# Performance work log

Measured on AMD Instinct MI355X. Metric: run time of the kernel, lower is better.

Reference implementation:

```python
import jax, jax.numpy as jnp
import numpy as np

DIM = 256
H = 4
K = 16
R = 4
EPS = 1e-5


def _conv1x1(x, W, b):
    # x: [B, Cin, N, P], W: [Cout, Cin], b: [Cout]
    return jnp.einsum('oc,bcnp->bonp', W, x) + b[None, :, None, None]


def setup_inputs() -> dict:
    key = jax.random.key(0)
    ks = jax.random.split(key, 12)
    B, N = 4, 8192
    s = 1.0 / np.sqrt(DIM)
    inp = {
        'queries': jax.random.normal(ks[0], (B, DIM, N, R), dtype=jnp.float32),
        'feats': jax.random.normal(ks[1], (B, DIM, N, K), dtype=jnp.float32),
        'Wq': jax.random.normal(ks[2], (DIM, DIM), dtype=jnp.float32) * s,
        'bq': jnp.zeros((DIM,), dtype=jnp.float32),
        'Wk': jax.random.normal(ks[3], (DIM, DIM), dtype=jnp.float32) * s,
        'bk': jnp.zeros((DIM,), dtype=jnp.float32),
        'Wv': jax.random.normal(ks[4], (DIM, DIM), dtype=jnp.float32) * s,
        'bv': jnp.zeros((DIM,), dtype=jnp.float32),
        'W1': jax.random.normal(ks[5], (2 * DIM, DIM), dtype=jnp.float32) * s,
        'b1': jnp.zeros((2 * DIM,), dtype=jnp.float32),
        'gamma': jnp.ones((2 * DIM,), dtype=jnp.float32),
        'beta': jnp.zeros((2 * DIM,), dtype=jnp.float32),
        'W2': jax.random.normal(ks[6], (DIM, 2 * DIM), dtype=jnp.float32) * (1.0 / np.sqrt(2 * DIM)),
        'b2': jnp.zeros((DIM,), dtype=jnp.float32),
    }
    return inp


def reference(queries, feats, Wq, bq, Wk, bk, Wv, bv, W1, b1, gamma, beta, W2, b2):
    B, _, N, _ = feats.shape
    d = DIM // H
    queries_iden = queries  # [B, dim, N, r]

    q = _conv1x1(queries, Wq, bq).reshape(B, H, d, N, R)   # [B,h,d,N,r]
    k = _conv1x1(feats, Wk, bk).reshape(B, H, d, N, K)     # [B,h,d,N,K]
    v = _conv1x1(feats, Wv, bv).reshape(B, H, d, N, K)     # [B,h,d,N,K]

    # logits: [B,N,h,r,K]
    logits = jnp.einsum('bhdnr,bhdnk->bnhrk', q, k) * (d ** -0.5)
    soft = jax.nn.softmax(logits, axis=-1)
    # agg: [B,N,h,r,d] -> permute to [B,N,h,d,r] -> [B,N,dim,r] -> [B,dim,N,r]
    agg = jnp.einsum('bnhrk,bhdnk->bnhdr', soft, v)
    agg = agg.reshape(B, N, DIM, R).transpose(0, 2, 1, 3)
    agg = agg + queries_iden

    # FFN: conv1x1 -> BN (training-mode batch stats) -> ReLU -> conv1x1, residual, ReLU
    h1 = _conv1x1(agg, W1, b1)  # [B, 2*dim, N, r]
    mean = jnp.mean(h1, axis=(0, 2, 3), keepdims=True)
    var = jnp.var(h1, axis=(0, 2, 3), keepdims=True)
    h1 = (h1 - mean) * jax.lax.rsqrt(var + EPS)
    h1 = h1 * gamma[None, :, None, None] + beta[None, :, None, None]
    h1 = jax.nn.relu(h1)
    h2 = _conv1x1(h1, W2, b2)
    return jax.nn.relu(h2 + agg)
```

## Files before the change

kernel.cpp:

```cpp
#include <hip/hip_runtime.h>
#include <hip/hip_bf16.h>

#define NB 4
#define NRQ 32768
#define NKF 131072

using u16 = unsigned short;
typedef short bf16x8 __attribute__((ext_vector_type(8)));
typedef float f32x4  __attribute__((ext_vector_type(4)));
typedef u16   u16x8  __attribute__((ext_vector_type(8)));
typedef u16   u16x4  __attribute__((ext_vector_type(4)));
typedef u16   u16x2  __attribute__((ext_vector_type(2)));

#if defined(__has_builtin)
#  if __has_builtin(__builtin_amdgcn_fdot2_f32_bf16)
#    define HAVE_DOT2 1
#  endif
#endif
#ifndef HAVE_DOT2
#  define HAVE_DOT2 0
#endif

#if HAVE_DOT2
typedef __bf16 bfv2 __attribute__((ext_vector_type(2)));
union bpack { bf16x8 v; bfv2 p[4]; };
__device__ __forceinline__ float dot2(bfv2 a, bfv2 b, float c){
  return __builtin_amdgcn_fdot2_f32_bf16(a, b, c, false);
}
#endif
union vpack { bf16x8 v; u16 e[8]; };

__device__ __forceinline__ u16 f2b(float f){
  unsigned u = __float_as_uint(f);
  return (u16)((u + 0x7fffu + ((u >> 16) & 1u)) >> 16);
}
__device__ __forceinline__ float b2f(u16 v){
  return __uint_as_float(((unsigned)v) << 16);
}

#define GLOAD16(g, l) __builtin_amdgcn_global_load_lds( \
    (const __attribute__((address_space(1))) unsigned int*)(g), \
    (__attribute__((address_space(3))) unsigned int*)(l), 16, 0, 0)

__global__ __launch_bounds__(256) void cvtW_k(
    const float* __restrict__ Wk, const float* __restrict__ Wv,
    const float* __restrict__ Wq, const float* __restrict__ W1,
    const float* __restrict__ W2, u16* __restrict__ wT)
{
  long e = ((long)blockIdx.x * 256 + threadIdx.x) * 8;
  const float* src; long off;
  if      (e < 65536)  { src = Wk; off = e; }
  else if (e < 131072) { src = Wv; off = e - 65536; }
  else if (e < 196608) { src = Wq; off = e - 131072; }
  else if (e < 327680) { src = W1; off = e - 196608; }
  else                 { src = W2; off = e - 327680; }
  float4 f0 = *reinterpret_cast<const float4*>(src + off);
  float4 f1 = *reinterpret_cast<const float4*>(src + off + 4);
  u16x8 p;
  p[0]=f2b(f0.x); p[1]=f2b(f0.y); p[2]=f2b(f0.z); p[3]=f2b(f0.w);
  p[4]=f2b(f1.x); p[5]=f2b(f1.y); p[6]=f2b(f1.z); p[7]=f2b(f1.w);
  *reinterpret_cast<u16x8*>(wT + e) = p;
}

__global__ void prep_k(const float* __restrict__ bk, const float* __restrict__ bv,
                       float* __restrict__ bKV, float* __restrict__ stats)
{
  int i = blockIdx.x * 256 + threadIdx.x;
  if (i < 512)       bKV[i] = (i < 256) ? bk[i] : bv[i - 256];
  else               stats[i - 512] = 0.f;
}

__global__ __launch_bounds__(256) void transpose_k(
    const float* __restrict__ in, u16* __restrict__ out,
    int NCtot, long outBatch)
{
  __shared__ u16 sT[64][264];
  const int t = threadIdx.x, b = blockIdx.y;
  const int nr0 = blockIdx.x * 64;
  const int cb = t >> 2, nrq = t & 3;
  const long ib = (long)b * 256 * NCtot + nr0;

  #pragma unroll
  for (int ci = 0; ci < 4; ++ci){
    const int c = cb + ci * 64;
    const float* src = in + ib + (long)c * NCtot + nrq * 16;
    #pragma unroll
    for (int j = 0; j < 4; ++j){
      float4 f = *reinterpret_cast<const float4*>(src + j * 4);
      int nr = nrq * 16 + j * 4;
      sT[nr+0][c] = f2b(f.x); sT[nr+1][c] = f2b(f.y);
      sT[nr+2][c] = f2b(f.z); sT[nr+3][c] = f2b(f.w);
    }
  }
  __syncthreads();
  const int row = t >> 2, qtr = t & 3;
  u16* orow = out + (long)b * outBatch + (long)(nr0 + row) * 256 + qtr * 64;
  #pragma unroll
  for (int i = 0; i < 8; ++i)
    *reinterpret_cast<u16x8*>(orow + i * 8) =
        *reinterpret_cast<const u16x8*>(&sT[row][qtr * 64 + i * 8]);
}

template<int MODE, int KD>
__global__ __launch_bounds__(256) void gemm_k(
    const u16* __restrict__ A, long aBatch, int chTiles,
    const u16* __restrict__ Wb, const float* __restrict__ bias,
    u16* __restrict__ outH, long oBatch, int NCH,
    float* __restrict__ statSum, float* __restrict__ statSq,
    const float* __restrict__ xsc, const float* __restrict__ xsh,
    const u16* __restrict__ residT,
    float* __restrict__ outF, long fBatch)
{
  __shared__ __align__(16) char sA[2][16384];
  __shared__ __align__(16) char sB[2][16384];

  const int t = threadIdx.x, lane = t & 63, wid = t >> 6;
  const int wm = wid >> 1, wn = wid & 1;
  const int b = blockIdx.z;

  const int nwg = gridDim.x, orig = blockIdx.x;
  const int qq = nwg >> 3, rr = nwg & 7, xcd = orig & 7, pos = orig >> 3;
  const int wg = (xcd < rr ? xcd * (qq + 1) : rr * (qq + 1) + (xcd - rr) * qq) + pos;
  const int rowT = wg / chTiles, chT = wg % chTiles;

  const u16* Ab = A + (long)b * aBatch + (long)rowT * 128 * KD;
  const u16* Wt = Wb + (long)chT * 128 * KD;
  const int sub = lane >> 3, kc8 = ((lane & 7) ^ sub) * 8;

  f32x4 acc[4][4];
  #pragma unroll
  for (int i = 0; i < 4; ++i)
    #pragma unroll
    for (int j = 0; j < 4; ++j) acc[i][j] = (f32x4){0.f,0.f,0.f,0.f};

  auto STAGE = [&](int buf, int ks){
    const int k0 = ks * 64;
    if constexpr (MODE == 3){
      const int wrow = t >> 1, whalf = t & 1;
      const u16* arow = Ab + (long)wrow * KD + k0 + whalf * 32;
      #pragma unroll
      for (int i = 0; i < 4; ++i){
        u16x8 v = *reinterpret_cast<const u16x8*>(arow + i * 8);
        const int kb = k0 + whalf*32 + i*8;
        float4 s0 = *reinterpret_cast<const float4*>(xsc + kb);
        float4 s1 = *reinterpret_cast<const float4*>(xsc + kb + 4);
        float4 h0 = *reinterpret_cast<const float4*>(xsh + kb);
        float4 h1 = *reinterpret_cast<const float4*>(xsh + kb + 4);
        u16x8 o;
        o[0]=f2b(fmaxf(b2f(v[0])*s0.x+h0.x,0.f));
        o[1]=f2b(fmaxf(b2f(v[1])*s0.y+h0.y,0.f));
        o[2]=f2b(fmaxf(b2f(v[2])*s0.z+h0.z,0.f));
        o[3]=f2b(fmaxf(b2f(v[3])*s0.w+h0.w,0.f));
        o[4]=f2b(fmaxf(b2f(v[4])*s1.x+h1.x,0.f));
        o[5]=f2b(fmaxf(b2f(v[5])*s1.y+h1.y,0.f));
        o[6]=f2b(fmaxf(b2f(v[6])*s1.z+h1.z,0.f));
        o[7]=f2b(fmaxf(b2f(v[7])*s1.w+h1.w,0.f));
        *reinterpret_cast<u16x8*>(
            sA[buf] + ((wrow*128 + whalf*64 + i*16) ^ ((wrow & 7) << 4))) = o;
      }
      #pragma unroll
      for (int i = 0; i < 4; ++i){
        const int chunk = wid * 4 + i;
        GLOAD16(Wt + (long)(chunk*8 + sub)*KD + k0 + kc8, sB[buf] + chunk*1024);
      }
    } else {
      #pragma unroll
      for (int i = 0; i < 4; ++i){
        const int chunk = wid * 4 + i;
        GLOAD16(Ab + (long)(chunk*8 + sub)*KD + k0 + kc8, sA[buf] + chunk*1024);
        GLOAD16(Wt + (long)(chunk*8 + sub)*KD + k0 + kc8, sB[buf] + chunk*1024);
      }
    }
  };

  constexpr int NT = KD / 64;
  STAGE(0, 0);
  __syncthreads();
  int cur = 0;
  for (int ks = 0; ks < NT; ++ks){
    if (ks + 1 < NT) STAGE(cur ^ 1, ks + 1);
    const char* pA = sA[cur]; const char* pB = sB[cur];
    #pragma unroll
    for (int kk = 0; kk < 2; ++kk){
      bf16x8 af[4], bf[4];
      #pragma unroll
      for (int mi = 0; mi < 4; ++mi){
        int m = wm*64 + mi*16 + (lane & 15);
        af[mi] = *reinterpret_cast<const bf16x8*>(
            pA + ((m*128 + kk*64 + (lane>>4)*16) ^ ((m & 7) << 4)));
      }
      #pragma unroll
      for (int ni = 0; ni < 4; ++ni){
        int c = wn*64 + ni*16 + (lane & 15);
        bf[ni] = *reinterpret_cast<const bf16x8*>(
            pB + ((c*128 + kk*64 + (lane>>4)*16) ^ ((c & 7) << 4)));
      }
      #pragma unroll
      for (int mi = 0; mi < 4; ++mi)
        #pragma unroll
        for (int ni = 0; ni < 4; ++ni)
          acc[mi][ni] = __builtin_amdgcn_mfma_f32_16x16x32_bf16(
              af[mi], bf[ni], acc[mi][ni], 0, 0, 0);
    }
    __syncthreads();
    cur ^= 1;
  }

  int chI[4]; float bv[4];
  #pragma unroll
  for (int ni = 0; ni < 4; ++ni){
    int ch = chT*128 + wn*64 + ni*16 + (lane & 15);
    chI[ni] = ch;
    bv[ni] = bias[ch];
  }
  if (MODE <= 1){
    float s[4] = {0,0,0,0}, sq[4] = {0,0,0,0};
    u16* outb = outH + (long)b * oBatch;
    #pragma unroll
    for (int mi = 0; mi < 4; ++mi){
      #pragma unroll
      for (int j = 0; j < 4; ++j){
        const long row = rowT*128 + wm*64 + mi*16 + (lane>>4)*4 + j;
        #pragma unroll
        for (int ni = 0; ni < 4; ++ni){
          float v = acc[mi][ni][j] + bv[ni];
          outb[row * NCH + chI[ni]] = f2b(v);
          if (MODE == 1){ s[ni] += v; sq[ni] += v * v; }
        }
      }
    }
    if (MODE == 1){
      #pragma unroll
      for (int ni = 0; ni < 4; ++ni){
        s[ni]  += __shfl_xor(s[ni], 16);  s[ni]  += __shfl_xor(s[ni], 32);
        sq[ni] += __shfl_xor(sq[ni], 16); sq[ni] += __shfl_xor(sq[ni], 32);
      }
      if (lane < 16){
        #pragma unroll
        for (int ni = 0; ni < 4; ++ni){
          atomicAdd(&statSum[chI[ni]], s[ni]);
          atomicAdd(&statSq[chI[ni]],  sq[ni]);
        }
      }
    }
  } else {
    const u16* rb = residT + (long)b * ((long)NRQ * 256);
    #pragma unroll
    for (int mi = 0; mi < 4; ++mi){
      const int nr0 = rowT*128 + wm*64 + mi*16 + (lane>>4)*4;
      #pragma unroll
      for (int ni = 0; ni < 4; ++ni){
        float4 o;
        o.x = fmaxf(acc[mi][ni][0] + bv[ni] + b2f(rb[(long)(nr0+0)*256 + chI[ni]]), 0.f);
        o.y = fmaxf(acc[mi][ni][1] + bv[ni] + b2f(rb[(long)(nr0+1)*256 + chI[ni]]), 0.f);
        o.z = fmaxf(acc[mi][ni][2] + bv[ni] + b2f(rb[(long)(nr0+2)*256 + chI[ni]]), 0.f);
        o.w = fmaxf(acc[mi][ni][3] + bv[ni] + b2f(rb[(long)(nr0+3)*256 + chI[ni]]), 0.f);
        *reinterpret_cast<float4*>(outF + (long)b*fBatch + (long)chI[ni]*NRQ + nr0) = o;
      }
    }
  }
}

__global__ __launch_bounds__(512, 4) void kvattn_k(
    const float* __restrict__ feats, const u16* __restrict__ wKV,
    const float* __restrict__ bKV, const u16* __restrict__ qT,
    const u16* __restrict__ qrT, u16* __restrict__ aggT)
{
  __shared__ __align__(16) char LDS[73728];
  char*  sAg = LDS;
  char*  sW  = LDS + 8192;
  char*  sK  = LDS;
  char*  sV  = LDS + 33792;
  float* sSf = (float*)(LDS + 67072);

  const int t = threadIdx.x, lane = t & 63, wid = t >> 6;
  const int wr = wid >> 2, wc = wid & 3;
  const int b = blockIdx.y;
  const long row0 = (long)blockIdx.x * 64;

  const int chL = t >> 4, nq = t & 15;
  const float* fbase = feats + (long)b * 256 * NKF + row0 + nq * 4;

  auto STAGEW = [&](int buf, int ks){
    const int k0 = ks * 32;
    #pragma unroll
    for (int i = 0; i < 4; ++i){
      const int cw = wid * 4 + i;
      const int ch = cw * 16 + (lane >> 2), jd = lane & 3;
      GLOAD16(wKV + (long)ch * 256 + k0 + ((jd ^ ((ch >> 1) & 3)) * 8),
              sW + buf * 32768 + cw * 1024);
    }
  };
  auto WRITEA = [&](int buf, float4 f){
    #pragma unroll
    for (int i = 0; i < 4; ++i){
      const int r = nq * 4 + i;
      const int byte = buf*4096 + r*64
                     + (((chL>>3) ^ ((r>>2)&3)) << 4) + (chL & 7)*2;
      float e = (i == 0) ? f.x : (i == 1) ? f.y : (i == 2) ? f.z : f.w;
      *reinterpret_cast<u16*>(sAg + byte) = f2b(e);
    }
  };

  f32x4 acc[2][8];
  #pragma unroll
  for (int i = 0; i < 2; ++i)
    #pragma unroll
    for (int j = 0; j < 8; ++j) acc[i][j] = (f32x4){0.f,0.f,0.f,0.f};

  {
    float4 a0 = *reinterpret_cast<const float4*>(fbase + (long)chL * NKF);
    STAGEW(0, 0);
    WRITEA(0, a0);
  }
  __syncthreads();
  int cur = 0;
  for (int ks = 0; ks < 8; ++ks){
    float4 an;
    if (ks < 7){
      an = *reinterpret_cast<const float4*>(fbase + (long)((ks+1)*32 + chL) * NKF);
      STAGEW(cur ^ 1, ks + 1);
    }
    const char* pA = sAg + cur * 4096;
    const char* pW = sW  + cur * 32768;
    bf16x8 af[2];
    #pragma unroll
    for (int mi = 0; mi < 2; ++mi){
      const int m = wr*32 + mi*16 + (lane & 15);
      af[mi] = *reinterpret_cast<const bf16x8*>(
          pA + m*64 + (((lane>>4) ^ ((m>>2)&3)) * 16));
    }
    #pragma unroll
    for (int ni = 0; ni < 8; ++ni){
      const int ch = wc*128 + ni*16 + (lane & 15);
      bf16x8 bf = *reinterpret_cast<const bf16x8*>(
          pW + ch*64 + (((lane>>4) ^ ((ch>>1)&3)) * 16));
      acc[0][ni] = __builtin_amdgcn_mfma_f32_16x16x32_bf16(af[0], bf, acc[0][ni], 0,0,0);
      acc[1][ni] = __builtin_amdgcn_mfma_f32_16x16x32_bf16(af[1], bf, acc[1][ni], 0,0,0);
    }
    if (ks < 7) WRITEA(cur ^ 1, an);
    __syncthreads();
    cur ^= 1;
  }

  {
    float bv[8];
    #pragma unroll
    for (int ni = 0; ni < 8; ++ni) bv[ni] = bKV[wc*128 + ni*16 + (lane & 15)];
    if (wc < 2){
      #pragma unroll
      for (int mi = 0; mi < 2; ++mi){
        const int p2 = wr*2 + mi;
        #pragma unroll
        for (int ni = 0; ni < 8; ++ni){
          const int ch = wc*128 + ni*16 + (lane & 15);
          #pragma unroll
          for (int j = 0; j < 4; ++j){
            const int kk2 = (lane>>4)*4 + j;
            *reinterpret_cast<u16*>(
                sK + (p2*16 + kk2)*528 + ((ch*2) ^ ((kk2 & 7) << 4))) =
                f2b(acc[mi][ni][j] + bv[ni]);
          }
        }
      }
    } else {
      #pragma unroll
      for (int mi = 0; mi < 2; ++mi){
        const int p2 = wr*2 + mi;
        #pragma unroll
        for (int ni = 0; ni < 8; ++ni){
          const int cv = (wc-2)*128 + ni*16 + (lane & 15);
          #pragma unroll
          for (int j = 0; j < 4; ++j){
            const int kk2 = (lane>>4)*4 + j;
            *reinterpret_cast<u16*>(sV + (p2*16 + kk2)*520 + cv*2) =
                f2b(acc[mi][ni][j] + bv[ni]);
          }
        }
      }
    }
  }
  __syncthreads();

  const int p = wid & 3, rh = wid >> 2;
  const int nqg = blockIdx.x * 4 + p;
  {
    const int h = lane >> 4, kk = lane & 15;
    const u16* qb = qT + ((long)b*NRQ + (long)nqg*4 + rh*2)*256 + h*64;
    const char* kr = sK + (p*16 + kk)*528;
    float l0 = 0.f, l1 = 0.f;
#if HAVE_DOT2
    #pragma unroll
    for (int d8 = 0; d8 < 8; ++d8){
      bpack K8, Q0, Q1;
      K8.v = *reinterpret_cast<const bf16x8*>(
          kr + ((h*128 + d8*16) ^ ((kk & 7) << 4)));
      Q0.v = *reinterpret_cast<const bf16x8*>(qb + d8*8);
      Q1.v = *reinterpret_cast<const bf16x8*>(qb + 256 + d8*8);
      #pragma unroll
      for (int pi = 0; pi < 4; ++pi){
        l0 = dot2(K8.p[pi], Q0.p[pi], l0);
        l1 = dot2(K8.p[pi], Q1.p[pi], l1);
      }
    }
#else
    #pragma unroll
    for (int d8 = 0; d8 < 8; ++d8){
      vpack K8, Q0, Q1;
      K8.v = *reinterpret_cast<const bf16x8*>(
          kr + ((h*128 + d8*16) ^ ((kk & 7) << 4)));
      Q0.v = *reinterpret_cast<const bf16x8*>(qb + d8*8);
      Q1.v = *reinterpret_cast<const bf16x8*>(qb + 256 + d8*8);
      #pragma unroll
      for (int e = 0; e < 8; ++e){
        float kf = b2f(K8.e[e]);
        l0 = fmaf(kf, b2f(Q0.e[e]), l0);
        l1 = fmaf(kf, b2f(Q1.e[e]), l1);
      }
    }
#endif
    float pr[2]; float lv[2] = {l0, l1};
    #pragma unroll
    for (int r = 0; r < 2; ++r){
      float x = lv[r] * 0.125f;
      float m = x;
      #pragma unroll
      for (int off = 1; off < 16; off <<= 1) m = fmaxf(m, __shfl_xor(m, off));
      float e = __expf(x - m);
      float ssum = e;
      #pragma unroll
      for (int off = 1; off < 16; off <<= 1) ssum += __shfl_xor(ssum, off);
      pr[r] = e / ssum;
    }
    *reinterpret_cast<float2*>(sSf + (p*4 + h)*68 + kk*4 + rh*2) =
        make_float2(pr[0], pr[1]);
  }
  __syncthreads();

  {
    const int c0 = rh*128 + lane*2;
    const int h = c0 >> 6;
    const char* vrow = sV + (p*16)*520;
    const float* ss = sSf + (p*4 + h)*68;
    float a[4][2] = {};
    #pragma unroll
    for (int kk = 0; kk < 16; ++kk){
      u16x2 vv = *reinterpret_cast<const u16x2*>(vrow + kk*520 + c0*2);
      float4 sv = *reinterpret_cast<const float4*>(ss + kk*4);
      float v0 = b2f(vv[0]), v1 = b2f(vv[1]);
      a[0][0] += sv.x*v0; a[0][1] += sv.x*v1;
      a[1][0] += sv.y*v0; a[1][1] += sv.y*v1;
      a[2][0] += sv.z*v0; a[2][1] += sv.z*v1;
      a[3][0] += sv.w*v0; a[3][1] += sv.w*v1;
    }
    const u16* rq = qrT + ((long)b*NRQ + (long)nqg*4)*256 + c0;
    u16* ob = aggT + ((long)b*NRQ + (long)nqg*4)*256 + c0;
    #pragma unroll
    for (int r = 0; r < 4; ++r){
      u16x2 q2 = *reinterpret_cast<const u16x2*>(rq + r*256);
      u16x2 pk;
      pk[0] = f2b(a[r][0] + b2f(q2[0]));
      pk[1] = f2b(a[r][1] + b2f(q2[1]));
      *reinterpret_cast<u16x2*>(ob + r*256) = pk;
    }
  }
}

__global__ void finalize_k(const float* __restrict__ st,
                           const float* __restrict__ gamma,
                           const float* __restrict__ beta,
                           float* __restrict__ out)
{
  int o = blockIdx.x*256 + threadIdx.x;
  const float inv = 1.f / 131072.f;
  float mean = st[o] * inv;
  float var  = st[512 + o] * inv - mean*mean;
  float sc   = gamma[o] * rsqrtf(var + 1e-5f);
  out[o]       = sc;
  out[512 + o] = beta[o] - mean * sc;
}

extern "C" void kernel_launch(void* const* d_in, const int* in_sizes, int n_in,
                              void* d_out, int out_size, void* d_ws, size_t ws_size,
                              hipStream_t stream)
{
  (void)in_sizes; (void)n_in; (void)out_size; (void)ws_size;
  const float* queries = (const float*)d_in[0];
  const float* feats   = (const float*)d_in[1];
  const float* Wq = (const float*)d_in[2];
  const float* bq = (const float*)d_in[3];
  const float* Wk = (const float*)d_in[4];
  const float* bk = (const float*)d_in[5];
  const float* Wv = (const float*)d_in[6];
  const float* bv = (const float*)d_in[7];
  const float* W1 = (const float*)d_in[8];
  const float* b1 = (const float*)d_in[9];
  const float* gamma = (const float*)d_in[10];
  const float* beta  = (const float*)d_in[11];
  const float* W2 = (const float*)d_in[12];
  const float* b2 = (const float*)d_in[13];

  char* ws = (char*)d_ws;
  u16*   h1T   = (u16*)ws;
  u16*   qrT   = (u16*)(ws + 134217728L);
  u16*   qT    = (u16*)(ws + 201326592L);
  u16*   aggT  = (u16*)(ws + 268435456L);
  float* stats = (float*)(ws + 335544320L);
  float* scale = stats + 1024;
  float* shift = stats + 1536;
  u16*   wT    = (u16*)(ws + 335552512L);
  u16*   wKV   = wT;
  u16*   wQ    = wT + 131072;
  u16*   wW1   = wT + 196608;
  u16*   wW2   = wT + 327680;
  float* bKV   = (float*)(wT + 458752);

  cvtW_k<<<dim3(224), 256, 0, stream>>>(Wk, Wv, Wq, W1, W2, wT);
  prep_k<<<dim3(6), 256, 0, stream>>>(bk, bv, bKV, stats);

  transpose_k<<<dim3(NRQ/64, NB), 256, 0, stream>>>(queries, qrT, NRQ, (long)NRQ*256);

  gemm_k<0, 256><<<dim3(512, 1, NB), 256, 0, stream>>>(
      qrT, (long)NRQ*256, 2, wQ, bq,
      qT, (long)NRQ*256, 256, nullptr, nullptr, nullptr, nullptr,
      nullptr, nullptr, 0);

  kvattn_k<<<dim3(NKF/64, NB), 512, 0, stream>>>(feats, wKV, bKV, qT, qrT, aggT);

  gemm_k<1, 256><<<dim3(1024, 1, NB), 256, 0, stream>>>(
      aggT, (long)NRQ*256, 4, wW1, b1,
      h1T, (long)NRQ*512, 512, stats, stats + 512, nullptr, nullptr,
      nullptr, nullptr, 0);

  finalize_k<<<dim3(2), 256, 0, stream>>>(stats, gamma, beta, scale);

  gemm_k<3, 512><<<dim3(512, 1, NB), 256, 0, stream>>>(
      h1T, (long)NRQ*512, 2, wW2, b2,
      nullptr, 0, 256, nullptr, nullptr, scale, shift,
      aggT, (float*)d_out, (long)256*NRQ);
}
```

Measured before the change: 649.3 us.

## Stage KV weights through registers with padded LDS, preload Q tile into LDS

Replaces the direct global-to-LDS double-buffered weight staging with register-prefetched loads stored into a single padded LDS buffer. The XOR-swizzled layouts for A, W and K are swapped for padded row strides. The Q rows for the block are loaded once into LDS with an async copy, so the attention step no longer reads them from global memory. In exchange, each k-step gets an extra barrier and register pressure rises. The padded layout uses narrower LDS accesses (4- and 8-byte), which may increase the LDS instruction count.

```diff
diff --git a/kernel.cpp b/kernel.cpp
--- a/kernel.cpp
+++ b/kernel.cpp
@@ -23,12 +23,15 @@
 
 #if HAVE_DOT2
 typedef __bf16 bfv2 __attribute__((ext_vector_type(2)));
-union bpack { bf16x8 v; bfv2 p[4]; };
+union bpack  { bf16x8 v; bfv2 p[4]; };
+union bpack4 { u16x4  v; bfv2 p[2]; };
 __device__ __forceinline__ float dot2(bfv2 a, bfv2 b, float c){
   return __builtin_amdgcn_fdot2_f32_bf16(a, b, c, false);
 }
 #endif
-union vpack { bf16x8 v; u16 e[8]; };
+union vpack  { bf16x8 v; u16 e[8]; };
+union wjoin  { u16x4 h[2]; bf16x8 v; u16x8 u; };
+union ajoin  { unsigned u[4]; bf16x8 v; };
 
 __device__ __forceinline__ u16 f2b(float f){
   unsigned u = __float_as_uint(f);
@@ -266,39 +269,46 @@
     const float* __restrict__ bKV, const u16* __restrict__ qT,
     const u16* __restrict__ qrT, u16* __restrict__ aggT)
 {
-  __shared__ __align__(16) char LDS[73728];
+  __shared__ __align__(16) char LDS[79104];
   char*  sAg = LDS;
-  char*  sW  = LDS + 8192;
+  char*  sW  = LDS + 8704;
   char*  sK  = LDS;
-  char*  sV  = LDS + 33792;
-  float* sSf = (float*)(LDS + 67072);
+  char*  sV  = LDS + 33280;
+  float* sSf = (float*)(LDS + 66560);
+  char*  sQ  = LDS + 70912;
 
   const int t = threadIdx.x, lane = t & 63, wid = t >> 6;
   const int wr = wid >> 2, wc = wid & 3;
   const int b = blockIdx.y;
   const long row0 = (long)blockIdx.x * 64;
 
+  GLOAD16(qT + ((long)b*NRQ + (long)blockIdx.x*16)*256 + wid*512 + lane*8,
+          sQ + wid*1024);
+
   const int chL = t >> 4, nq = t & 15;
   const float* fbase = feats + (long)b * 256 * NKF + row0 + nq * 4;
-
-  auto STAGEW = [&](int buf, int ks){
-    const int k0 = ks * 32;
+  const int wch0 = t >> 2, wslot = t & 3;
+
+  auto LOADW = [&](int ks, wjoin* wreg){
+    #pragma unroll
+    for (int i = 0; i < 4; ++i)
+      wreg[i].u = *reinterpret_cast<const u16x8*>(
+          wKV + (long)(wch0 + i*128) * 256 + ks*32 + wslot*8);
+  };
+  auto STOREW = [&](wjoin* wreg){
     #pragma unroll
     for (int i = 0; i < 4; ++i){
-      const int cw = wid * 4 + i;
-      const int ch = cw * 16 + (lane >> 2), jd = lane & 3;
-      GLOAD16(wKV + (long)ch * 256 + k0 + ((jd ^ ((ch >> 1) & 3)) * 8),
-              sW + buf * 32768 + cw * 1024);
+      char* base = sW + (wch0 + i*128)*72 + wslot*16;
+      *reinterpret_cast<u16x4*>(base)     = wreg[i].h[0];
+      *reinterpret_cast<u16x4*>(base + 8) = wreg[i].h[1];
     }
   };
   auto WRITEA = [&](int buf, float4 f){
     #pragma unroll
     for (int i = 0; i < 4; ++i){
-      const int r = nq * 4 + i;
-      const int byte = buf*4096 + r*64
-                     + (((chL>>3) ^ ((r>>2)&3)) << 4) + (chL & 7)*2;
+      const int r = nq*4 + i;
       float e = (i == 0) ? f.x : (i == 1) ? f.y : (i == 2) ? f.z : f.w;
-      *reinterpret_cast<u16*>(sAg + byte) = f2b(e);
+      *reinterpret_cast<u16*>(sAg + buf*4352 + r*68 + chL*2) = f2b(e);
     }
   };
 
@@ -309,37 +319,51 @@
     for (int j = 0; j < 8; ++j) acc[i][j] = (f32x4){0.f,0.f,0.f,0.f};
 
   {
+    wjoin w0[4];
+    LOADW(0, w0);
     float4 a0 = *reinterpret_cast<const float4*>(fbase + (long)chL * NKF);
-    STAGEW(0, 0);
+    STOREW(w0);
     WRITEA(0, a0);
   }
   __syncthreads();
+
   int cur = 0;
+  const int jq = lane >> 4;
   for (int ks = 0; ks < 8; ++ks){
-    float4 an;
+    wjoin wnext[4]; float4 an;
     if (ks < 7){
+      LOADW(ks + 1, wnext);
       an = *reinterpret_cast<const float4*>(fbase + (long)((ks+1)*32 + chL) * NKF);
-      STAGEW(cur ^ 1, ks + 1);
-    }
-    const char* pA = sAg + cur * 4096;
-    const char* pW = sW  + cur * 32768;
+    }
+    const char* pA = sAg + cur * 4352;
     bf16x8 af[2];
     #pragma unroll
     for (int mi = 0; mi < 2; ++mi){
       const int m = wr*32 + mi*16 + (lane & 15);
-      af[mi] = *reinterpret_cast<const bf16x8*>(
-          pA + m*64 + (((lane>>4) ^ ((m>>2)&3)) * 16));
+      const char* ab = pA + m*68 + jq*16;
+      ajoin A_;
+      A_.u[0] = *reinterpret_cast<const unsigned*>(ab);
+      A_.u[1] = *reinterpret_cast<const unsigned*>(ab + 4);
+      A_.u[2] = *reinterpret_cast<const unsigned*>(ab + 8);
+      A_.u[3] = *reinterpret_cast<const unsigned*>(ab + 12);
+      af[mi] = A_.v;
     }
     #pragma unroll
     for (int ni = 0; ni < 8; ++ni){
       const int ch = wc*128 + ni*16 + (lane & 15);
-      bf16x8 bf = *reinterpret_cast<const bf16x8*>(
-          pW + ch*64 + (((lane>>4) ^ ((ch>>1)&3)) * 16));
-      acc[0][ni] = __builtin_amdgcn_mfma_f32_16x16x32_bf16(af[0], bf, acc[0][ni], 0,0,0);
-      acc[1][ni] = __builtin_amdgcn_mfma_f32_16x16x32_bf16(af[1], bf, acc[1][ni], 0,0,0);
+      const char* wb = sW + ch*72 + jq*16;
+      wjoin B_;
+      B_.h[0] = *reinterpret_cast<const u16x4*>(wb);
+      B_.h[1] = *reinterpret_cast<const u16x4*>(wb + 8);
+      acc[0][ni] = __builtin_amdgcn_mfma_f32_16x16x32_bf16(af[0], B_.v, acc[0][ni], 0,0,0);
+      acc[1][ni] = __builtin_amdgcn_mfma_f32_16x16x32_bf16(af[1], B_.v, acc[1][ni], 0,0,0);
     }
     if (ks < 7) WRITEA(cur ^ 1, an);
     __syncthreads();
+    if (ks < 7){
+      STOREW(wnext);
+      __syncthreads();
+    }
     cur ^= 1;
   }
 
@@ -347,35 +371,19 @@
     float bv[8];
     #pragma unroll
     for (int ni = 0; ni < 8; ++ni) bv[ni] = bKV[wc*128 + ni*16 + (lane & 15)];
-    if (wc < 2){
-      #pragma unroll
-      for (int mi = 0; mi < 2; ++mi){
-        const int p2 = wr*2 + mi;
+    char* dst = (wc < 2) ? sK : sV;
+    const int chb = (wc & 1) * 128;
+    #pragma unroll
+    for (int mi = 0; mi < 2; ++mi){
+      const int p2 = wr*2 + mi;
+      #pragma unroll
+      for (int ni = 0; ni < 8; ++ni){
+        const int ch = chb + ni*16 + (lane & 15);
         #pragma unroll
-        for (int ni = 0; ni < 8; ++ni){
-          const int ch = wc*128 + ni*16 + (lane & 15);
-          #pragma unroll
-          for (int j = 0; j < 4; ++j){
-            const int kk2 = (lane>>4)*4 + j;
-            *reinterpret_cast<u16*>(
-                sK + (p2*16 + kk2)*528 + ((ch*2) ^ ((kk2 & 7) << 4))) =
-                f2b(acc[mi][ni][j] + bv[ni]);
-          }
-        }
-      }
-    } else {
-      #pragma unroll
-      for (int mi = 0; mi < 2; ++mi){
-        const int p2 = wr*2 + mi;
-        #pragma unroll
-        for (int ni = 0; ni < 8; ++ni){
-          const int cv = (wc-2)*128 + ni*16 + (lane & 15);
-          #pragma unroll
-          for (int j = 0; j < 4; ++j){
-            const int kk2 = (lane>>4)*4 + j;
-            *reinterpret_cast<u16*>(sV + (p2*16 + kk2)*520 + cv*2) =
-                f2b(acc[mi][ni][j] + bv[ni]);
-          }
+        for (int j = 0; j < 4; ++j){
+          const int kk2 = (lane>>4)*4 + j;
+          *reinterpret_cast<u16*>(dst + (p2*16 + kk2)*520 + ch*2) =
+              f2b(acc[mi][ni][j] + bv[ni]);
         }
       }
     }
@@ -386,31 +394,30 @@
   const int nqg = blockIdx.x * 4 + p;
   {
     const int h = lane >> 4, kk = lane & 15;
-    const u16* qb = qT + ((long)b*NRQ + (long)nqg*4 + rh*2)*256 + h*64;
-    const char* kr = sK + (p*16 + kk)*528;
+    const char* kr = sK + (p*16 + kk)*520 + h*128;
+    const char* q0r = sQ + (p*4 + rh*2)*512 + h*128;
     float l0 = 0.f, l1 = 0.f;
 #if HAVE_DOT2
     #pragma unroll
     for (int d8 = 0; d8 < 8; ++d8){
-      bpack K8, Q0, Q1;
-      K8.v = *reinterpret_cast<const bf16x8*>(
-          kr + ((h*128 + d8*16) ^ ((kk & 7) << 4)));
-      Q0.v = *reinterpret_cast<const bf16x8*>(qb + d8*8);
-      Q1.v = *reinterpret_cast<const bf16x8*>(qb + 256 + d8*8);
-      #pragma unroll
-      for (int pi = 0; pi < 4; ++pi){
-        l0 = dot2(K8.p[pi], Q0.p[pi], l0);
-        l1 = dot2(K8.p[pi], Q1.p[pi], l1);
-      }
+      bpack4 klo, khi;
+      klo.v = *reinterpret_cast<const u16x4*>(kr + d8*16);
+      khi.v = *reinterpret_cast<const u16x4*>(kr + d8*16 + 8);
+      bpack Q0, Q1;
+      Q0.v = *reinterpret_cast<const bf16x8*>(q0r + d8*16);
+      Q1.v = *reinterpret_cast<const bf16x8*>(q0r + 512 + d8*16);
+      l0 = dot2(klo.p[0], Q0.p[0], l0); l0 = dot2(klo.p[1], Q0.p[1], l0);
+      l0 = dot2(khi.p[0], Q0.p[2], l0); l0 = dot2(khi.p[1], Q0.p[3], l0);
+      l1 = dot2(klo.p[0], Q1.p[0], l1); l1 = dot2(klo.p[1], Q1.p[1], l1);
+      l1 = dot2(khi.p[0], Q1.p[2], l1); l1 = dot2(khi.p[1], Q1.p[3], l1);
     }
 #else
     #pragma unroll
     for (int d8 = 0; d8 < 8; ++d8){
       vpack K8, Q0, Q1;
-      K8.v = *reinterpret_cast<const bf16x8*>(
-          kr + ((h*128 + d8*16) ^ ((kk & 7) << 4)));
-      Q0.v = *reinterpret_cast<const bf16x8*>(qb + d8*8);
-      Q1.v = *reinterpret_cast<const bf16x8*>(qb + 256 + d8*8);
+      K8.v = *reinterpret_cast<const bf16x8*>(kr + d8*16);
+      Q0.v = *reinterpret_cast<const bf16x8*>(q0r + d8*16);
+      Q1.v = *reinterpret_cast<const bf16x8*>(q0r + 512 + d8*16);
       #pragma unroll
       for (int e = 0; e < 8; ++e){
         float kf = b2f(K8.e[e]);
```

Measured after the change: 791.4 us. 1.22x slower.

## Fuse queries transpose into Q-projection GEMM and read fp32 residual directly

Applied to the files above, without the earlier changes.

Removes the standalone transpose kernel that converted queries to a bf16 row-major copy. The Q-projection GEMM gains a MODE 4 that loads fp32 queries in channel-major order, converts them to bf16 and writes them into swizzled LDS. The attention kernel now reads the fp32 queries for its residual add, and the bias/stats prep kernel is merged into the weight-conversion kernel as extra blocks. This saves a full pass over the queries plus one intermediate buffer and two launches. The cost is scalar 2-byte LDS stores in the GEMM A-stage, and the residual now uses unrounded fp32 values.

```diff
diff --git a/kernel.cpp b/kernel.cpp
--- a/kernel.cpp
+++ b/kernel.cpp
@@ -45,8 +45,16 @@
 __global__ __launch_bounds__(256) void cvtW_k(
     const float* __restrict__ Wk, const float* __restrict__ Wv,
     const float* __restrict__ Wq, const float* __restrict__ W1,
-    const float* __restrict__ W2, u16* __restrict__ wT)
+    const float* __restrict__ W2, u16* __restrict__ wT,
+    const float* __restrict__ bk, const float* __restrict__ bv,
+    float* __restrict__ bKV, float* __restrict__ stats)
 {
+  if (blockIdx.x >= 224){
+    int i = (blockIdx.x - 224) * 256 + threadIdx.x;
+    if (i < 512)       bKV[i] = (i < 256) ? bk[i] : bv[i - 256];
+    else if (i < 1536) stats[i - 512] = 0.f;
+    return;
+  }
   long e = ((long)blockIdx.x * 256 + threadIdx.x) * 8;
   const float* src; long off;
   if      (e < 65536)  { src = Wk; off = e; }
@@ -62,45 +70,6 @@
   *reinterpret_cast<u16x8*>(wT + e) = p;
 }
 
-__global__ void prep_k(const float* __restrict__ bk, const float* __restrict__ bv,
-                       float* __restrict__ bKV, float* __restrict__ stats)
-{
-  int i = blockIdx.x * 256 + threadIdx.x;
-  if (i < 512)       bKV[i] = (i < 256) ? bk[i] : bv[i - 256];
-  else               stats[i - 512] = 0.f;
-}
-
-__global__ __launch_bounds__(256) void transpose_k(
-    const float* __restrict__ in, u16* __restrict__ out,
-    int NCtot, long outBatch)
-{
-  __shared__ u16 sT[64][264];
-  const int t = threadIdx.x, b = blockIdx.y;
-  const int nr0 = blockIdx.x * 64;
-  const int cb = t >> 2, nrq = t & 3;
-  const long ib = (long)b * 256 * NCtot + nr0;
-
-  #pragma unroll
-  for (int ci = 0; ci < 4; ++ci){
-    const int c = cb + ci * 64;
-    const float* src = in + ib + (long)c * NCtot + nrq * 16;
-    #pragma unroll
-    for (int j = 0; j < 4; ++j){
-      float4 f = *reinterpret_cast<const float4*>(src + j * 4);
-      int nr = nrq * 16 + j * 4;
-      sT[nr+0][c] = f2b(f.x); sT[nr+1][c] = f2b(f.y);
-      sT[nr+2][c] = f2b(f.z); sT[nr+3][c] = f2b(f.w);
-    }
-  }
-  __syncthreads();
-  const int row = t >> 2, qtr = t & 3;
-  u16* orow = out + (long)b * outBatch + (long)(nr0 + row) * 256 + qtr * 64;
-  #pragma unroll
-  for (int i = 0; i < 8; ++i)
-    *reinterpret_cast<u16x8*>(orow + i * 8) =
-        *reinterpret_cast<const u16x8*>(&sT[row][qtr * 64 + i * 8]);
-}
-
 template<int MODE, int KD>
 __global__ __launch_bounds__(256) void gemm_k(
     const u16* __restrict__ A, long aBatch, int chTiles,
@@ -108,6 +77,7 @@
     u16* __restrict__ outH, long oBatch, int NCH,
     float* __restrict__ statSum, float* __restrict__ statSq,
     const float* __restrict__ xsc, const float* __restrict__ xsh,
+    const float* __restrict__ Afp,
     const u16* __restrict__ residT,
     float* __restrict__ outF, long fBatch)
 {
@@ -163,6 +133,26 @@
         const int chunk = wid * 4 + i;
         GLOAD16(Wt + (long)(chunk*8 + sub)*KD + k0 + kc8, sB[buf] + chunk*1024);
       }
+    } else if constexpr (MODE == 4){
+      const int chq = lane;
+      const float* qsrc = Afp + (long)b * aBatch
+                        + (long)(k0 + chq) * NRQ + rowT * 128 + wid * 32;
+      #pragma unroll
+      for (int i = 0; i < 8; ++i){
+        float4 f = *reinterpret_cast<const float4*>(qsrc + i * 4);
+        #pragma unroll
+        for (int j = 0; j < 4; ++j){
+          const int m = wid*32 + i*4 + j;
+          float e = (j == 0) ? f.x : (j == 1) ? f.y : (j == 2) ? f.z : f.w;
+          *reinterpret_cast<u16*>(
+              sA[buf] + ((m*128 + chq*2) ^ ((m & 7) << 4))) = f2b(e);
+        }
+      }
+      #pragma unroll
+      for (int i = 0; i < 4; ++i){
+        const int chunk = wid * 4 + i;
+        GLOAD16(Wt + (long)(chunk*8 + sub)*KD + k0 + kc8, sB[buf] + chunk*1024);
+      }
     } else {
       #pragma unroll
       for (int i = 0; i < 4; ++i){
@@ -213,7 +203,7 @@
     chI[ni] = ch;
     bv[ni] = bias[ch];
   }
-  if (MODE <= 1){
+  if (MODE != 3){
     float s[4] = {0,0,0,0}, sq[4] = {0,0,0,0};
     u16* outb = outH + (long)b * oBatch;
     #pragma unroll
@@ -264,7 +254,7 @@
 __global__ __launch_bounds__(512, 4) void kvattn_k(
     const float* __restrict__ feats, const u16* __restrict__ wKV,
     const float* __restrict__ bKV, const u16* __restrict__ qT,
-    const u16* __restrict__ qrT, u16* __restrict__ aggT)
+    const float* __restrict__ queriesF, u16* __restrict__ aggT)
 {
   __shared__ __align__(16) char LDS[73728];
   char*  sAg = LDS;
@@ -453,14 +443,17 @@
       a[2][0] += sv.z*v0; a[2][1] += sv.z*v1;
       a[3][0] += sv.w*v0; a[3][1] += sv.w*v1;
     }
-    const u16* rq = qrT + ((long)b*NRQ + (long)nqg*4)*256 + c0;
+    const float* qf = queriesF + ((long)b*256 + c0) * NRQ + (long)nqg*4;
+    float4 q0 = *reinterpret_cast<const float4*>(qf);
+    float4 q1 = *reinterpret_cast<const float4*>(qf + NRQ);
+    const float* q0a = (const float*)&q0;
+    const float* q1a = (const float*)&q1;
     u16* ob = aggT + ((long)b*NRQ + (long)nqg*4)*256 + c0;
     #pragma unroll
     for (int r = 0; r < 4; ++r){
-      u16x2 q2 = *reinterpret_cast<const u16x2*>(rq + r*256);
       u16x2 pk;
-      pk[0] = f2b(a[r][0] + b2f(q2[0]));
-      pk[1] = f2b(a[r][1] + b2f(q2[1]));
+      pk[0] = f2b(a[r][0] + q0a[r]);
+      pk[1] = f2b(a[r][1] + q1a[r]);
       *reinterpret_cast<u16x2*>(ob + r*256) = pk;
     }
   }
@@ -502,7 +495,6 @@
 
   char* ws = (char*)d_ws;
   u16*   h1T   = (u16*)ws;
-  u16*   qrT   = (u16*)(ws + 134217728L);
   u16*   qT    = (u16*)(ws + 201326592L);
   u16*   aggT  = (u16*)(ws + 268435456L);
   float* stats = (float*)(ws + 335544320L);
@@ -515,27 +507,26 @@
   u16*   wW2   = wT + 327680;
   float* bKV   = (float*)(wT + 458752);
 
-  cvtW_k<<<dim3(224), 256, 0, stream>>>(Wk, Wv, Wq, W1, W2, wT);
-  prep_k<<<dim3(6), 256, 0, stream>>>(bk, bv, bKV, stats);
-
-  transpose_k<<<dim3(NRQ/64, NB), 256, 0, stream>>>(queries, qrT, NRQ, (long)NRQ*256);
-
-  gemm_k<0, 256><<<dim3(512, 1, NB), 256, 0, stream>>>(
-      qrT, (long)NRQ*256, 2, wQ, bq,
+  cvtW_k<<<dim3(230), 256, 0, stream>>>(Wk, Wv, Wq, W1, W2, wT,
+                                        bk, bv, bKV, stats);
+
+  gemm_k<4, 256><<<dim3(512, 1, NB), 256, 0, stream>>>(
+      qT, (long)256*NRQ, 2, wQ, bq,
       qT, (long)NRQ*256, 256, nullptr, nullptr, nullptr, nullptr,
-      nullptr, nullptr, 0);
-
-  kvattn_k<<<dim3(NKF/64, NB), 512, 0, stream>>>(feats, wKV, bKV, qT, qrT, aggT);
+      queries, nullptr, nullptr, 0);
+
+  kvattn_k<<<dim3(NKF/64, NB), 512, 0, stream>>>(
+      feats, wKV, bKV, qT, queries, aggT);
 
   gemm_k<1, 256><<<dim3(1024, 1, NB), 256, 0, stream>>>(
       aggT, (long)NRQ*256, 4, wW1, b1,
       h1T, (long)NRQ*512, 512, stats, stats + 512, nullptr, nullptr,
-      nullptr, nullptr, 0);
+      nullptr, nullptr, nullptr, 0);
 
   finalize_k<<<dim3(2), 256, 0, stream>>>(stats, gamma, beta, scale);
 
   gemm_k<3, 512><<<dim3(512, 1, NB), 256, 0, stream>>>(
       h1T, (long)NRQ*512, 2, wW2, b2,
       nullptr, 0, 256, nullptr, nullptr, scale, shift,
-      aggT, (float*)d_out, (long)256*NRQ);
-}
+      nullptr, aggT, (float*)d_out, (long)256*NRQ);
+}
```

Result: slower. 666.0 us (+2.6%).
